# Kernel optimization log

Measured on AMD Instinct MI355X. Metric: run time of the kernel, lower is better.

## Reference

```python
import jax, jax.numpy as jnp
import numpy as np

NB, H = 4, 8          # blocks, heads
B, S = 2, 1024        # batch, seq
D, HID = 512, 512     # input_dim, hidden_dim (must match, see zeros_like(x) branch)
# mod computed from neurochem BEFORE _modulate_neurochem, using init values
MOD = 0.5 * 1.1 + 0.5 * 0.7 + 0.5 * 1.3 - 0.0 * 1.2  # = 1.55


def setup_inputs() -> dict:
    key = jax.random.key(0)
    ks = jax.random.split(key, 12)
    sc = 1.0 / np.sqrt(D)
    inp = {
        "x": jax.random.normal(ks[0], (B, S, D), jnp.float32),
        "Wq": jax.random.normal(ks[1], (NB, D, HID), jnp.float32) * sc,
        "bq": jax.random.normal(ks[2], (NB, HID), jnp.float32) * sc,
        "Wk": jax.random.normal(ks[3], (NB, D, HID), jnp.float32) * sc,
        "bk": jax.random.normal(ks[4], (NB, HID), jnp.float32) * sc,
        "Wv": jax.random.normal(ks[5], (NB, D, HID), jnp.float32) * sc,
        "bv": jax.random.normal(ks[6], (NB, HID), jnp.float32) * sc,
        "Wo": jax.random.normal(ks[7], (NB, HID, D), jnp.float32) * sc,
        "bo": jax.random.normal(ks[8], (NB, D), jnp.float32) * sc,
        "strength": jax.random.uniform(ks[9], (NB, H, H), jnp.float32),
        # gate = (osc_mask * spike_mask > 0.5) materialized as 0/1 floats
        "gate": (jax.random.uniform(ks[10], (NB, H)) < 0.7).astype(jnp.float32),
    }
    return inp


def reference(x, Wq, bq, Wk, bk, Wv, bv, Wo, bo, strength, gate):
    # per-block projections (shared across heads in the original loop)
    q = jnp.einsum('bsd,ndh->nbsh', x, Wq) + bq[:, None, None, :]
    k = jnp.einsum('bsd,ndh->nbsh', x, Wk) + bk[:, None, None, :]
    v = jnp.einsum('bsd,ndh->nbsh', x, Wv) + bv[:, None, None, :]
    scores = jnp.einsum('nbsh,nbth->nbst', q, k) / jnp.sqrt(jnp.float32(HID))
    # per-head scalar bias: diagonal synaptic strength, clamped
    s = jnp.clip(jnp.diagonal(strength, axis1=1, axis2=2), 0.01, 1.0)  # [NB, H]
    scaled = scores[:, None] * s[:, :, None, None, None]  # [NB, H, B, S, S]
    probs = jax.nn.softmax(scaled, axis=-1)
    # head outputs summed with the 0/1 osc*spike gate
    head_sum = jnp.einsum('nhbst,nbtd,nh->nbsd', probs, v, gate)  # [NB, B, S, HID]
    block_out = jnp.einsum('nbsd,ndo->nbso', head_sum, Wo) + bo[:, None, None, :]
    return block_out.sum(axis=0) * jnp.float32(MOD)
```

## Files before the change

kernel.cpp:

```cpp
#include <hip/hip_runtime.h>
#include <math.h>

#define NBLK   4
#define NH     8
#define BATCH  2
#define SEQ    1024
#define DIM    512
#define HIDDEN 512
#define MODF   1.55f
#define INV_SQRT_HID 0.04419417382415922f

typedef __bf16 bf16;
typedef __bf16 bf16x4 __attribute__((ext_vector_type(4)));
typedef __bf16 bf16x8 __attribute__((ext_vector_type(8)));
typedef float  floatx4 __attribute__((ext_vector_type(4)));

constexpr int BM = 128, BN = 128, BK = 32;

__device__ __forceinline__ void load16_lds(const bf16* g, bf16* l) {
    __builtin_amdgcn_global_load_lds(
        (__attribute__((address_space(1))) void*)g,
        (__attribute__((address_space(3))) void*)l, 16, 0, 0);
}

__device__ __forceinline__ void stage32(
    const bf16* __restrict__ Ab, int lda,
    const bf16* __restrict__ Bb, int ldb, int k0,
    bf16* As, bf16* Bs, int w, int l)
{
    const int s0 = 2 * w, s1 = s0 + 1;
    const int r0 = s0 * 16 + (l >> 2);
    const int r1 = s1 * 16 + (l >> 2);
    const int kc = (l & 3) * 8;
    load16_lds(Ab + (size_t)r0 * lda + k0 + kc, As + s0 * 512);
    load16_lds(Ab + (size_t)r1 * lda + k0 + kc, As + s1 * 512);
    load16_lds(Bb + (size_t)r0 * ldb + k0 + kc, Bs + s0 * 512);
    load16_lds(Bb + (size_t)r1 * ldb + k0 + kc, Bs + s1 * 512);
}

__device__ __forceinline__ void comp32(
    const bf16* As, const bf16* Bs,
    int wr, int wc, int fr, int fk, floatx4 (&acc)[4][4])
{
    bf16x8 af[4], bg[4];
#pragma unroll
    for (int i = 0; i < 4; ++i)
        af[i] = *(const bf16x8*)&As[(wr + i * 16 + fr) * BK + fk];
#pragma unroll
    for (int j = 0; j < 4; ++j)
        bg[j] = *(const bf16x8*)&Bs[(wc + j * 16 + fr) * BK + fk];
#pragma unroll
    for (int i = 0; i < 4; ++i)
#pragma unroll
        for (int j = 0; j < 4; ++j)
            acc[i][j] = __builtin_amdgcn_mfma_f32_16x16x32_bf16(
                af[i], bg[j], acc[i][j], 0, 0, 0);
}

__device__ __forceinline__ void mfma_nt4(
    const bf16* __restrict__ A, int lda,
    const bf16* __restrict__ B, int ldb,
    int K, int m0, int n0, floatx4 (&acc)[4][4])
{
    __shared__ __align__(16) bf16 As0[BM * BK];
    __shared__ __align__(16) bf16 Bs0[BN * BK];
    __shared__ __align__(16) bf16 As1[BM * BK];
    __shared__ __align__(16) bf16 Bs1[BN * BK];

    const int tid = threadIdx.x;
    const int l   = tid & 63;
    const int w   = tid >> 6;
    const int wr  = (w >> 1) * 64;
    const int wc  = (w & 1) * 64;
    const int fr  = l & 15;
    const int fk  = (l >> 4) * 8;

    const bf16* Ab = A + (size_t)m0 * lda;
    const bf16* Bb = B + (size_t)n0 * ldb;

    const int nIter = K / BK;
    stage32(Ab, lda, Bb, ldb, 0, As0, Bs0, w, l);
    for (int k = 0; k < nIter; k += 2) {
        __syncthreads();
        if (k + 1 < nIter)
            stage32(Ab, lda, Bb, ldb, (k + 1) * BK, As1, Bs1, w, l);
        comp32(As0, Bs0, wr, wc, fr, fk, acc);
        __syncthreads();
        if (k + 2 < nIter)
            stage32(Ab, lda, Bb, ldb, (k + 2) * BK, As0, Bs0, w, l);
        comp32(As1, Bs1, wr, wc, fr, fk, acc);
    }
}

__device__ __forceinline__ void stage8(
    const bf16* __restrict__ Ab, int lda,
    const bf16* __restrict__ Bb, int ldb, int k0,
    bf16* As, bf16* Bs, int w, int l)
{
    const int row = w * 16 + (l >> 2);
    const int kc  = (l & 3) * 8;
    load16_lds(Ab + (size_t)row * lda + k0 + kc, As + w * 512);
    load16_lds(Bb + (size_t)row * ldb + k0 + kc, Bs + w * 512);
}

__device__ __forceinline__ void comp8(
    const bf16* As, const bf16* Bs,
    int wr, int wc, int fr, int fk, floatx4 (&acc)[4][2])
{
    bf16x8 af[4], bg[2];
#pragma unroll
    for (int i = 0; i < 4; ++i)
        af[i] = *(const bf16x8*)&As[(wr + i * 16 + fr) * BK + fk];
#pragma unroll
    for (int j = 0; j < 2; ++j)
        bg[j] = *(const bf16x8*)&Bs[(wc + j * 16 + fr) * BK + fk];
#pragma unroll
    for (int i = 0; i < 4; ++i)
#pragma unroll
        for (int j = 0; j < 2; ++j)
            acc[i][j] = __builtin_amdgcn_mfma_f32_16x16x32_bf16(
                af[i], bg[j], acc[i][j], 0, 0, 0);
}

__device__ __forceinline__ void mfma_nt8(
    const bf16* __restrict__ A, int lda,
    const bf16* __restrict__ B, int ldb,
    int K, int m0, int n0, floatx4 (&acc)[4][2])
{
    __shared__ __align__(16) bf16 As0[BM * BK];
    __shared__ __align__(16) bf16 Bs0[BN * BK];
    __shared__ __align__(16) bf16 As1[BM * BK];
    __shared__ __align__(16) bf16 Bs1[BN * BK];

    const int tid = threadIdx.x;
    const int l   = tid & 63;
    const int w   = tid >> 6;
    const int wr  = (w >> 2) * 64;
    const int wc  = (w & 3) * 32;
    const int fr  = l & 15;
    const int fk  = (l >> 4) * 8;

    const bf16* Ab = A + (size_t)m0 * lda;
    const bf16* Bb = B + (size_t)n0 * ldb;

    const int nIter = K / BK;
    stage8(Ab, lda, Bb, ldb, 0, As0, Bs0, w, l);
    for (int k = 0; k < nIter; k += 2) {
        __syncthreads();
        if (k + 1 < nIter)
            stage8(Ab, lda, Bb, ldb, (k + 1) * BK, As1, Bs1, w, l);
        comp8(As0, Bs0, wr, wc, fr, fk, acc);
        __syncthreads();
        if (k + 2 < nIter)
            stage8(Ab, lda, Bb, ldb, (k + 2) * BK, As0, Bs0, w, l);
        comp8(As1, Bs1, wr, wc, fr, fk, acc);
    }
}

__global__ __launch_bounds__(256) void xconv_kernel(
    const float* __restrict__ x, bf16* __restrict__ xb)
{
    const int t = blockIdx.x * 256 + threadIdx.x;
    const float4 v = ((const float4*)x)[t];
    bf16x4 o = { (bf16)v.x, (bf16)v.y, (bf16)v.z, (bf16)v.w };
    *(bf16x4*)&xb[(size_t)t * 4] = o;
}

__global__ __launch_bounds__(256) void transpose_w_kernel(
    const float* __restrict__ Wq, const float* __restrict__ Wk,
    const float* __restrict__ Wv, const float* __restrict__ Wo,
    bf16* __restrict__ WqT, bf16* __restrict__ WkT,
    bf16* __restrict__ WvT, bf16* __restrict__ WoT)
{
    __shared__ float tile[32][33];
    const int z = blockIdx.z;
    const int mat = z >> 2, n = z & 3;
    const float* src; bf16* dst;
    if (mat == 0)      { src = Wq; dst = WqT; }
    else if (mat == 1) { src = Wk; dst = WkT; }
    else if (mat == 2) { src = Wv; dst = WvT; }
    else               { src = Wo; dst = WoT; }
    src += (size_t)n * 512 * 512;
    dst += (size_t)n * 512 * 512;

    const int tx = threadIdx.x & 31, ty = threadIdx.x >> 5;
    const int x0 = blockIdx.x * 32, y0 = blockIdx.y * 32;
#pragma unroll
    for (int r = 0; r < 4; ++r)
        tile[ty + r * 8][tx] = src[(size_t)(y0 + ty + r * 8) * 512 + x0 + tx];
    __syncthreads();
#pragma unroll
    for (int r = 0; r < 4; ++r)
        dst[(size_t)(x0 + ty + r * 8) * 512 + y0 + tx] = (bf16)tile[tx][ty + r * 8];
}

__global__ __launch_bounds__(256) void proj_mfma_kernel(
    const bf16* __restrict__ xb,
    const bf16* __restrict__ WqT, const bf16* __restrict__ WkT,
    const bf16* __restrict__ WvT,
    const float* __restrict__ bq, const float* __restrict__ bk,
    const float* __restrict__ bv,
    bf16* __restrict__ Qh, bf16* __restrict__ Kh, bf16* __restrict__ Vt)
{
    const int z = blockIdx.z;
    const int n = z & 3, which = z >> 2;
    const bf16* WT; const float* bias;
    if (which == 0)      { WT = WqT; bias = bq; }
    else if (which == 1) { WT = WkT; bias = bk; }
    else                 { WT = WvT; bias = bv; }
    WT   += (size_t)n * DIM * HIDDEN;
    bias += (size_t)n * HIDDEN;

    const int m0 = blockIdx.y * BM, n0 = blockIdx.x * BN;
    floatx4 acc[4][4] = {};
    mfma_nt4(xb, DIM, WT, DIM, DIM, m0, n0, acc);

    const int l = threadIdx.x & 63, w = threadIdx.x >> 6;
    const int rb = m0 + (w >> 1) * 64 + (l >> 4) * 4;
    const int cb = n0 + (w & 1) * 64 + (l & 15);

    if (which != 2) {
        bf16* C = (which ? Kh : Qh) + (size_t)n * (BATCH * SEQ) * HIDDEN;
#pragma unroll
        for (int j = 0; j < 4; ++j) {
            const int col = cb + j * 16;
            const float bc = bias[col];
#pragma unroll
            for (int i = 0; i < 4; ++i)
#pragma unroll
                for (int r = 0; r < 4; ++r)
                    C[(size_t)(rb + i * 16 + r) * HIDDEN + col] = (bf16)(acc[i][j][r] + bc);
        }
    } else {
        const int b = m0 >> 10;
        bf16* Cv = Vt + (size_t)(n * BATCH + b) * HIDDEN * SEQ;
        const int tb = rb & (SEQ - 1);
#pragma unroll
        for (int j = 0; j < 4; ++j) {
            const int col = cb + j * 16;
            const float bc = bias[col];
#pragma unroll
            for (int i = 0; i < 4; ++i) {
                bf16x4 o = { (bf16)(acc[i][j][0] + bc), (bf16)(acc[i][j][1] + bc),
                             (bf16)(acc[i][j][2] + bc), (bf16)(acc[i][j][3] + bc) };
                *(bf16x4*)&Cv[(size_t)col * SEQ + tb + i * 16] = o;
            }
        }
    }
}

__global__ __launch_bounds__(512) void scores_mfma_kernel(
    const bf16* __restrict__ Qh, const bf16* __restrict__ Kh,
    float* __restrict__ P)
{
    const int z = blockIdx.z;
    const bf16* A = Qh + (size_t)z * SEQ * HIDDEN;
    const bf16* B = Kh + (size_t)z * SEQ * HIDDEN;
    float* C = P + (size_t)z * SEQ * SEQ;

    const int m0 = blockIdx.y * BM, n0 = blockIdx.x * BN;
    floatx4 acc[4][2] = {};
    mfma_nt8(A, HIDDEN, B, HIDDEN, HIDDEN, m0, n0, acc);

    const int l = threadIdx.x & 63, w = threadIdx.x >> 6;
    const int rb = m0 + (w >> 2) * 64 + (l >> 4) * 4;
    const int cb = n0 + (w & 3) * 32 + (l & 15);
#pragma unroll
    for (int i = 0; i < 4; ++i)
#pragma unroll
        for (int j = 0; j < 2; ++j)
#pragma unroll
            for (int r = 0; r < 4; ++r)
                C[(size_t)(rb + i * 16 + r) * SEQ + cb + j * 16] =
                    acc[i][j][r] * INV_SQRT_HID;
}

__global__ __launch_bounds__(256) void softmax_combine_kernel(
    const float* __restrict__ P, bf16* __restrict__ Pb,
    const float* __restrict__ strength, const float* __restrict__ gate)
{
    const int row = blockIdx.x;
    const int n = row >> 11;
    const float* prow = P + (size_t)row * SEQ;
    const int tid = threadIdx.x;
    const int wid = tid >> 6, lane = tid & 63;

    float4 v = ((const float4*)prow)[tid];

    float m = fmaxf(fmaxf(v.x, v.y), fmaxf(v.z, v.w));
#pragma unroll
    for (int off = 32; off > 0; off >>= 1) m = fmaxf(m, __shfl_down(m, off));
    __shared__ float redm[4];
    if (lane == 0) redm[wid] = m;
    __syncthreads();
    const float M = fmaxf(fmaxf(redm[0], redm[1]), fmaxf(redm[2], redm[3]));

    float sh[NH], gh[NH];
#pragma unroll
    for (int h = 0; h < NH; ++h) {
        sh[h] = fminf(fmaxf(strength[n * NH * NH + h * NH + h], 0.01f), 1.0f);
        gh[h] = gate[n * NH + h];
    }

    const float e[4] = { v.x - M, v.y - M, v.z - M, v.w - M };
    float E[4][NH];
    float zsum[NH];
#pragma unroll
    for (int h = 0; h < NH; ++h) zsum[h] = 0.f;
#pragma unroll
    for (int i = 0; i < 4; ++i)
#pragma unroll
        for (int h = 0; h < NH; ++h) {
            const float t = __expf(sh[h] * e[i]);
            E[i][h] = t; zsum[h] += t;
        }

#pragma unroll
    for (int h = 0; h < NH; ++h)
#pragma unroll
        for (int off = 32; off > 0; off >>= 1) zsum[h] += __shfl_down(zsum[h], off);
    __shared__ float redz[4][NH];
    if (lane == 0)
#pragma unroll
        for (int h = 0; h < NH; ++h) redz[wid][h] = zsum[h];
    __syncthreads();

    float wgt[NH];
#pragma unroll
    for (int h = 0; h < NH; ++h) {
        const float Z = redz[0][h] + redz[1][h] + redz[2][h] + redz[3][h];
        wgt[h] = gh[h] / Z;
    }

    bf16x4 o;
#pragma unroll
    for (int i = 0; i < 4; ++i) {
        float s = 0.f;
#pragma unroll
        for (int h = 0; h < NH; ++h) s += wgt[h] * E[i][h];
        o[i] = (bf16)s;
    }
    *(bf16x4*)&Pb[(size_t)row * SEQ + tid * 4] = o;
}

__global__ __launch_bounds__(512) void pv_mfma_kernel(
    const bf16* __restrict__ Pb, const bf16* __restrict__ Vt,
    bf16* __restrict__ HS)
{
    const int z = blockIdx.z;
    const bf16* A = Pb + (size_t)z * SEQ * SEQ;
    const bf16* B = Vt + (size_t)z * HIDDEN * SEQ;
    bf16* C = HS + (size_t)z * SEQ * HIDDEN;

    const int m0 = blockIdx.y * BM, n0 = blockIdx.x * BN;
    floatx4 acc[4][2] = {};
    mfma_nt8(A, SEQ, B, SEQ, SEQ, m0, n0, acc);

    const int l = threadIdx.x & 63, w = threadIdx.x >> 6;
    const int rb = m0 + (w >> 2) * 64 + (l >> 4) * 4;
    const int cb = n0 + (w & 3) * 32 + (l & 15);
#pragma unroll
    for (int i = 0; i < 4; ++i)
#pragma unroll
        for (int j = 0; j < 2; ++j)
#pragma unroll
            for (int r = 0; r < 4; ++r)
                C[(size_t)(rb + i * 16 + r) * HIDDEN + cb + j * 16] =
                    (bf16)acc[i][j][r];
}

__global__ __launch_bounds__(512) void out_partial_kernel(
    const bf16* __restrict__ HS, const bf16* __restrict__ WoT,
    float* __restrict__ Opart)
{
    const int n = blockIdx.z;
    const bf16* A = HS + (size_t)n * (BATCH * SEQ) * HIDDEN;
    const bf16* B = WoT + (size_t)n * HIDDEN * DIM;
    float* C = Opart + (size_t)n * (BATCH * SEQ) * DIM;

    const int m0 = blockIdx.y * BM, n0 = blockIdx.x * BN;
    floatx4 acc[4][2] = {};
    mfma_nt8(A, HIDDEN, B, HIDDEN, HIDDEN, m0, n0, acc);

    const int l = threadIdx.x & 63, w = threadIdx.x >> 6;
    const int rb = m0 + (w >> 2) * 64 + (l >> 4) * 4;
    const int cb = n0 + (w & 3) * 32 + (l & 15);
#pragma unroll
    for (int i = 0; i < 4; ++i)
#pragma unroll
        for (int j = 0; j < 2; ++j)
#pragma unroll
            for (int r = 0; r < 4; ++r)
                C[(size_t)(rb + i * 16 + r) * DIM + cb + j * 16] = acc[i][j][r];
}

__global__ __launch_bounds__(256) void out_reduce_kernel(
    const float* __restrict__ Opart, const float* __restrict__ bo,
    float* __restrict__ out)
{
    const size_t t = (size_t)blockIdx.x * 256 + threadIdx.x;
    const int c = (int)((t * 4) & (DIM - 1));
    const size_t stride4 = (size_t)(BATCH * SEQ) * DIM / 4;

    float4 s = ((const float4*)Opart)[t];
#pragma unroll
    for (int n = 1; n < NBLK; ++n) {
        const float4 p = ((const float4*)Opart)[t + n * stride4];
        s.x += p.x; s.y += p.y; s.z += p.z; s.w += p.w;
    }
    float4 bs = make_float4(0.f, 0.f, 0.f, 0.f);
#pragma unroll
    for (int n = 0; n < NBLK; ++n) {
        const float4 b = *(const float4*)(bo + n * DIM + c);
        bs.x += b.x; bs.y += b.y; bs.z += b.z; bs.w += b.w;
    }
    ((float4*)out)[t] = make_float4((s.x + bs.x) * MODF, (s.y + bs.y) * MODF,
                                    (s.z + bs.z) * MODF, (s.w + bs.w) * MODF);
}

extern "C" void kernel_launch(void* const* d_in, const int* in_sizes, int n_in,
                              void* d_out, int out_size, void* d_ws, size_t ws_size,
                              hipStream_t stream) {
    const float* x        = (const float*)d_in[0];
    const float* Wq       = (const float*)d_in[1];
    const float* bq       = (const float*)d_in[2];
    const float* Wk       = (const float*)d_in[3];
    const float* bk       = (const float*)d_in[4];
    const float* Wv       = (const float*)d_in[5];
    const float* bv       = (const float*)d_in[6];
    const float* Wo       = (const float*)d_in[7];
    const float* bo       = (const float*)d_in[8];
    const float* strength = (const float*)d_in[9];
    const float* gate     = (const float*)d_in[10];
    float* out = (float*)d_out;

    char* ws = (char*)d_ws;
    bf16*  xb    = (bf16*)(ws);
    bf16*  WqT   = (bf16*)(ws + (2u  << 20));
    bf16*  WkT   = (bf16*)(ws + (4u  << 20));
    bf16*  WvT   = (bf16*)(ws + (6u  << 20));
    bf16*  WoT   = (bf16*)(ws + (8u  << 20));
    bf16*  Qh    = (bf16*)(ws + (10u << 20));
    bf16*  Kh    = (bf16*)(ws + (18u << 20));
    bf16*  Vt    = (bf16*)(ws + (26u << 20));
    float* Pf    = (float*)(ws + (34u << 20));
    bf16*  Pb    = (bf16*)(ws + (10u << 20));
    bf16*  HS    = (bf16*)(ws + (34u << 20));
    float* Opart = (float*)(ws + (42u << 20));

    xconv_kernel<<<dim3((BATCH * SEQ * DIM) / 1024), 256, 0, stream>>>(x, xb);
    transpose_w_kernel<<<dim3(16, 16, 16), 256, 0, stream>>>(
        Wq, Wk, Wv, Wo, WqT, WkT, WvT, WoT);

    proj_mfma_kernel<<<dim3(HIDDEN / BN, (BATCH * SEQ) / BM, 3 * NBLK), 256, 0, stream>>>(
        xb, WqT, WkT, WvT, bq, bk, bv, Qh, Kh, Vt);

    scores_mfma_kernel<<<dim3(SEQ / BN, SEQ / BM, NBLK * BATCH), 512, 0, stream>>>(
        Qh, Kh, Pf);

    softmax_combine_kernel<<<dim3(NBLK * BATCH * SEQ), 256, 0, stream>>>(
        Pf, Pb, strength, gate);

    pv_mfma_kernel<<<dim3(HIDDEN / BN, SEQ / BM, NBLK * BATCH), 512, 0, stream>>>(
        Pb, Vt, HS);

    out_partial_kernel<<<dim3(DIM / BN, (BATCH * SEQ) / BM, NBLK), 512, 0, stream>>>(
        HS, WoT, Opart);

    out_reduce_kernel<<<dim3((BATCH * SEQ) * DIM / 4 / 256), 256, 0, stream>>>(
        Opart, bo, out);
}
```

Measured before the change: 189.1 us.

## Double GEMM K-tile to 64, merge prep kernels, skip gated-off heads in softmax

Templates the shared MFMA GEMM mainloop on its K-tile depth and uses 64 instead of 32 for the scores, PV and output GEMMs. This halves the number of barriers and staging rounds per block at the cost of twice the LDS per block. The x-to-bf16 conversion is merged into the weight transpose kernel as an extra grid slice, saving one launch. The softmax-combine kernel now skips the exp, reduction and accumulation for heads whose gate is zero, which is a data-dependent branch on the gate input.

Result: no change. 190.7 us (+0.9%).

```diff
diff --git a/kernel.cpp b/kernel.cpp
--- a/kernel.cpp
+++ b/kernel.cpp
@@ -92,45 +92,59 @@
     }
 }
 
-__device__ __forceinline__ void stage8(
+template<int BKT>
+__device__ __forceinline__ void stage8T(
     const bf16* __restrict__ Ab, int lda,
     const bf16* __restrict__ Bb, int ldb, int k0,
     bf16* As, bf16* Bs, int w, int l)
 {
-    const int row = w * 16 + (l >> 2);
-    const int kc  = (l & 3) * 8;
-    load16_lds(Ab + (size_t)row * lda + k0 + kc, As + w * 512);
-    load16_lds(Bb + (size_t)row * ldb + k0 + kc, Bs + w * 512);
-}
-
-__device__ __forceinline__ void comp8(
+    constexpr int NL  = BKT / 32;
+    constexpr int RPS = 512 / BKT;
+    constexpr int CPL = BKT / 8;
+#pragma unroll
+    for (int i = 0; i < NL; ++i) {
+        const int seg = w * NL + i;
+        const int row = seg * RPS + l / CPL;
+        const int kc  = (l % CPL) * 8;
+        load16_lds(Ab + (size_t)row * lda + k0 + kc, As + seg * 512);
+        load16_lds(Bb + (size_t)row * ldb + k0 + kc, Bs + seg * 512);
+    }
+}
+
+template<int BKT>
+__device__ __forceinline__ void comp8T(
     const bf16* As, const bf16* Bs,
     int wr, int wc, int fr, int fk, floatx4 (&acc)[4][2])
 {
-    bf16x8 af[4], bg[2];
-#pragma unroll
-    for (int i = 0; i < 4; ++i)
-        af[i] = *(const bf16x8*)&As[(wr + i * 16 + fr) * BK + fk];
-#pragma unroll
-    for (int j = 0; j < 2; ++j)
-        bg[j] = *(const bf16x8*)&Bs[(wc + j * 16 + fr) * BK + fk];
-#pragma unroll
-    for (int i = 0; i < 4; ++i)
+#pragma unroll
+    for (int ks = 0; ks < BKT / 32; ++ks) {
+        const int ko = ks * 32 + fk;
+        bf16x8 af[4], bg[2];
+#pragma unroll
+        for (int i = 0; i < 4; ++i)
+            af[i] = *(const bf16x8*)&As[(wr + i * 16 + fr) * BKT + ko];
 #pragma unroll
         for (int j = 0; j < 2; ++j)
-            acc[i][j] = __builtin_amdgcn_mfma_f32_16x16x32_bf16(
-                af[i], bg[j], acc[i][j], 0, 0, 0);
-}
-
+            bg[j] = *(const bf16x8*)&Bs[(wc + j * 16 + fr) * BKT + ko];
+#pragma unroll
+        for (int i = 0; i < 4; ++i)
+#pragma unroll
+            for (int j = 0; j < 2; ++j)
+                acc[i][j] = __builtin_amdgcn_mfma_f32_16x16x32_bf16(
+                    af[i], bg[j], acc[i][j], 0, 0, 0);
+    }
+}
+
+template<int BKT>
 __device__ __forceinline__ void mfma_nt8(
     const bf16* __restrict__ A, int lda,
     const bf16* __restrict__ B, int ldb,
     int K, int m0, int n0, floatx4 (&acc)[4][2])
 {
-    __shared__ __align__(16) bf16 As0[BM * BK];
-    __shared__ __align__(16) bf16 Bs0[BN * BK];
-    __shared__ __align__(16) bf16 As1[BM * BK];
-    __shared__ __align__(16) bf16 Bs1[BN * BK];
+    __shared__ __align__(16) bf16 As0[BM * BKT];
+    __shared__ __align__(16) bf16 Bs0[BN * BKT];
+    __shared__ __align__(16) bf16 As1[BM * BKT];
+    __shared__ __align__(16) bf16 Bs1[BN * BKT];
 
     const int tid = threadIdx.x;
     const int l   = tid & 63;
@@ -143,37 +157,42 @@
     const bf16* Ab = A + (size_t)m0 * lda;
     const bf16* Bb = B + (size_t)n0 * ldb;
 
-    const int nIter = K / BK;
-    stage8(Ab, lda, Bb, ldb, 0, As0, Bs0, w, l);
+    const int nIter = K / BKT;
+    stage8T<BKT>(Ab, lda, Bb, ldb, 0, As0, Bs0, w, l);
     for (int k = 0; k < nIter; k += 2) {
         __syncthreads();
         if (k + 1 < nIter)
-            stage8(Ab, lda, Bb, ldb, (k + 1) * BK, As1, Bs1, w, l);
-        comp8(As0, Bs0, wr, wc, fr, fk, acc);
+            stage8T<BKT>(Ab, lda, Bb, ldb, (k + 1) * BKT, As1, Bs1, w, l);
+        comp8T<BKT>(As0, Bs0, wr, wc, fr, fk, acc);
         __syncthreads();
         if (k + 2 < nIter)
-            stage8(Ab, lda, Bb, ldb, (k + 2) * BK, As0, Bs0, w, l);
-        comp8(As1, Bs1, wr, wc, fr, fk, acc);
-    }
-}
-
-__global__ __launch_bounds__(256) void xconv_kernel(
-    const float* __restrict__ x, bf16* __restrict__ xb)
-{
-    const int t = blockIdx.x * 256 + threadIdx.x;
-    const float4 v = ((const float4*)x)[t];
-    bf16x4 o = { (bf16)v.x, (bf16)v.y, (bf16)v.z, (bf16)v.w };
-    *(bf16x4*)&xb[(size_t)t * 4] = o;
-}
-
-__global__ __launch_bounds__(256) void transpose_w_kernel(
+            stage8T<BKT>(Ab, lda, Bb, ldb, (k + 2) * BKT, As0, Bs0, w, l);
+        comp8T<BKT>(As1, Bs1, wr, wc, fr, fk, acc);
+    }
+}
+
+__global__ __launch_bounds__(256) void prep_kernel(
+    const float* __restrict__ x,
     const float* __restrict__ Wq, const float* __restrict__ Wk,
     const float* __restrict__ Wv, const float* __restrict__ Wo,
+    bf16* __restrict__ xb,
     bf16* __restrict__ WqT, bf16* __restrict__ WkT,
     bf16* __restrict__ WvT, bf16* __restrict__ WoT)
 {
+    const int z = blockIdx.z;
+    if (z == 16) {
+        const int bid = blockIdx.y * 16 + blockIdx.x;
+        const int base = bid * 1024 + threadIdx.x;
+#pragma unroll
+        for (int i = 0; i < 4; ++i) {
+            const int idx = base + i * 256;
+            const float4 v = ((const float4*)x)[idx];
+            bf16x4 o = { (bf16)v.x, (bf16)v.y, (bf16)v.z, (bf16)v.w };
+            *(bf16x4*)&xb[(size_t)idx * 4] = o;
+        }
+        return;
+    }
     __shared__ float tile[32][33];
-    const int z = blockIdx.z;
     const int mat = z >> 2, n = z & 3;
     const float* src; bf16* dst;
     if (mat == 0)      { src = Wq; dst = WqT; }
@@ -260,7 +279,7 @@
 
     const int m0 = blockIdx.y * BM, n0 = blockIdx.x * BN;
     floatx4 acc[4][2] = {};
-    mfma_nt8(A, HIDDEN, B, HIDDEN, HIDDEN, m0, n0, acc);
+    mfma_nt8<64>(A, HIDDEN, B, HIDDEN, HIDDEN, m0, n0, acc);
 
     const int l = threadIdx.x & 63, w = threadIdx.x >> 6;
     const int rb = m0 + (w >> 2) * 64 + (l >> 4) * 4;
@@ -308,26 +327,29 @@
 #pragma unroll
     for (int h = 0; h < NH; ++h) zsum[h] = 0.f;
 #pragma unroll
-    for (int i = 0; i < 4; ++i)
-#pragma unroll
-        for (int h = 0; h < NH; ++h) {
+    for (int h = 0; h < NH; ++h) {
+        if (gh[h] == 0.f) continue;
+#pragma unroll
+        for (int i = 0; i < 4; ++i) {
             const float t = __expf(sh[h] * e[i]);
             E[i][h] = t; zsum[h] += t;
         }
-
-#pragma unroll
-    for (int h = 0; h < NH; ++h)
+    }
+
+    __shared__ float redz[4][NH];
+#pragma unroll
+    for (int h = 0; h < NH; ++h) {
+        if (gh[h] == 0.f) continue;
 #pragma unroll
         for (int off = 32; off > 0; off >>= 1) zsum[h] += __shfl_down(zsum[h], off);
-    __shared__ float redz[4][NH];
-    if (lane == 0)
-#pragma unroll
-        for (int h = 0; h < NH; ++h) redz[wid][h] = zsum[h];
+        if (lane == 0) redz[wid][h] = zsum[h];
+    }
     __syncthreads();
 
     float wgt[NH];
 #pragma unroll
     for (int h = 0; h < NH; ++h) {
+        if (gh[h] == 0.f) { wgt[h] = 0.f; continue; }
         const float Z = redz[0][h] + redz[1][h] + redz[2][h] + redz[3][h];
         wgt[h] = gh[h] / Z;
     }
@@ -337,7 +359,8 @@
     for (int i = 0; i < 4; ++i) {
         float s = 0.f;
 #pragma unroll
-        for (int h = 0; h < NH; ++h) s += wgt[h] * E[i][h];
+        for (int h = 0; h < NH; ++h)
+            if (gh[h] != 0.f) s += wgt[h] * E[i][h];
         o[i] = (bf16)s;
     }
     *(bf16x4*)&Pb[(size_t)row * SEQ + tid * 4] = o;
@@ -354,7 +377,7 @@
 
     const int m0 = blockIdx.y * BM, n0 = blockIdx.x * BN;
     floatx4 acc[4][2] = {};
-    mfma_nt8(A, SEQ, B, SEQ, SEQ, m0, n0, acc);
+    mfma_nt8<64>(A, SEQ, B, SEQ, SEQ, m0, n0, acc);
 
     const int l = threadIdx.x & 63, w = threadIdx.x >> 6;
     const int rb = m0 + (w >> 2) * 64 + (l >> 4) * 4;
@@ -380,7 +403,7 @@
 
     const int m0 = blockIdx.y * BM, n0 = blockIdx.x * BN;
     floatx4 acc[4][2] = {};
-    mfma_nt8(A, HIDDEN, B, HIDDEN, HIDDEN, m0, n0, acc);
+    mfma_nt8<64>(A, HIDDEN, B, HIDDEN, HIDDEN, m0, n0, acc);
 
     const int l = threadIdx.x & 63, w = threadIdx.x >> 6;
     const int rb = m0 + (w >> 2) * 64 + (l >> 4) * 4;
@@ -448,9 +471,8 @@
     bf16*  HS    = (bf16*)(ws + (34u << 20));
     float* Opart = (float*)(ws + (42u << 20));
 
-    xconv_kernel<<<dim3((BATCH * SEQ * DIM) / 1024), 256, 0, stream>>>(x, xb);
-    transpose_w_kernel<<<dim3(16, 16, 16), 256, 0, stream>>>(
-        Wq, Wk, Wv, Wo, WqT, WkT, WvT, WoT);
+    prep_kernel<<<dim3(16, 16, 17), 256, 0, stream>>>(
+        x, Wq, Wk, Wv, Wo, xb, WqT, WkT, WvT, WoT);
 
     proj_mfma_kernel<<<dim3(HIDDEN / BN, (BATCH * SEQ) / BM, 3 * NBLK), 256, 0, stream>>>(
         xb, WqT, WkT, WvT, bq, bk, bv, Qh, Kh, Vt);
```
